# Kernel tuning notes

Measured on AMD Instinct MI355X. Metric: run time of the kernel, lower is better.

The kernel has to match this reference:

```python
import jax, jax.numpy as jnp
import numpy as np

ALPHA = 0.5  # config_param['alpha']


def setup_inputs() -> dict:
    key = jax.random.key(0)
    ks = jax.random.split(key, 10)
    B, T, N, E, H = 64, 20, 8192, 128, 128
    # sparse multi-hot basket indicators
    x = (jax.random.uniform(ks[0], (B, T, N)) < 0.01).astype(jnp.float32)
    seq_len = jax.random.randint(ks[1], (B,), 1, T + 1)  # pack_padded requires >=1
    A = jax.random.uniform(ks[2], (N, N), dtype=jnp.float32) * 0.01  # dense item-item adjacency
    W1 = jax.random.normal(ks[3], (E, N), dtype=jnp.float32) * 0.02
    b1 = jnp.zeros((E,), jnp.float32)
    W2 = jax.random.normal(ks[4], (E, N), dtype=jnp.float32) * 0.02
    b2 = jnp.zeros((E,), jnp.float32)
    W_ih = jax.random.normal(ks[5], (4 * H, E), dtype=jnp.float32) * 0.05
    W_hh = jax.random.normal(ks[6], (4 * H, H), dtype=jnp.float32) * 0.05
    b_ih = jnp.zeros((4 * H,), jnp.float32)
    b_hh = jnp.zeros((4 * H,), jnp.float32)
    W_out = jax.random.normal(ks[7], (N, H), dtype=jnp.float32) * 0.02
    I_B = jnp.ones((N,), jnp.float32) / N  # item_probs-style bias init
    threshold = jnp.array([0.005], jnp.float32)  # adj_matrix.mean()
    return dict(x=x, seq_len=seq_len, A=A, W1=W1, b1=b1, W2=W2, b2=b2,
                W_ih=W_ih, W_hh=W_hh, b_ih=b_ih, b_hh=b_hh,
                W_out=W_out, I_B=I_B, threshold=threshold)


def reference(x, seq_len, A, W1, b1, W2, b2, W_ih, W_hh, b_ih, b_hh, W_out, I_B, threshold):
    B, T, N = x.shape
    H = W_hh.shape[1]
    xf = x.reshape(B * T, N)
    # two basket encoders, elementwise max combine (dropout = identity in eval)
    e1 = jax.nn.relu(xf @ W1.T + b1)
    e2 = jax.nn.relu(xf @ W2.T + b2)
    basket = jnp.maximum(e1, e2).reshape(B, T, -1)  # [B, T, E]

    # 1-layer LSTM (torch gate order i,f,g,o); packed variable-length seqs
    # emulated by freezing (h, c) once t >= seq_len, so h_n matches pack_padded.
    valid = jnp.arange(T)[:, None] < seq_len[None, :]  # [T, B]
    xs = basket.transpose(1, 0, 2)                     # [T, B, E]
    b = b_ih + b_hh

    def step(carry, inp):
        h, c = carry
        x_t, v = inp
        gates = x_t @ W_ih.T + h @ W_hh.T + b
        i, f, g, o = jnp.split(gates, 4, axis=-1)
        c_new = jax.nn.sigmoid(f) * c + jax.nn.sigmoid(i) * jnp.tanh(g)
        h_new = jax.nn.sigmoid(o) * jnp.tanh(c_new)
        m = v[:, None]
        return (jnp.where(m, h_new, h), jnp.where(m, c_new, c)), None

    h0 = jnp.zeros((B, H), x.dtype)
    c0 = jnp.zeros((B, H), x.dtype)
    (h_n, _), _ = jax.lax.scan(step, (h0, c0), (xs, valid))

    p = jax.nn.sigmoid(h_n @ W_out.T)  # [B, N]
    # mm(p, diag(relu(I_B))) is algebraically an elementwise scale
    predict = (1.0 - ALPHA) * p + ALPHA * (p * jax.nn.relu(I_B) + jax.nn.relu(p @ A))
    return predict
```

## Files before the change

### kernel.cpp

```cpp
#include <hip/hip_runtime.h>
#include <hip/hip_bf16.h>
#include <stdint.h>

#define B_ 64
#define T_ 20
#define N_ 8192
#define E_ 128
#define H_ 128
#define G4 512
#define SPLITK 8

typedef short bf16x8 __attribute__((ext_vector_type(8)));
typedef float f32x4 __attribute__((ext_vector_type(4)));

__device__ __forceinline__ float sigmoidf_(float x){ return 1.0f/(1.0f+expf(-x)); }

__device__ __forceinline__ unsigned short f2bf(float f){
  union { float f; uint32_t u; } v; v.f = f;
  uint32_t u = v.u;
  uint32_t r = (u + 0x7FFFu + ((u >> 16) & 1u)) >> 16;
  return (unsigned short)r;
}
__device__ __forceinline__ uint32_t pk2(float a, float b){
  return (uint32_t)f2bf(a) | ((uint32_t)f2bf(b) << 16);
}
__device__ __forceinline__ float bf2f(unsigned short s){
  union { uint32_t u; float f; } v; v.u = ((uint32_t)s) << 16; return v.f;
}

__global__ void k_transpose(const float* __restrict__ W1, const float* __restrict__ W2,
                            unsigned short* __restrict__ W12T){
  __shared__ float t1[128][33];
  __shared__ float t2[128][33];
  int n0 = blockIdx.x * 32;
  int tid = threadIdx.x;
  int nl = tid & 31, eg = tid >> 5;
  for (int i = 0; i < 16; i++){
    int e = eg * 16 + i;
    t1[e][nl] = W1[(size_t)e*N_ + n0 + nl];
    t2[e][nl] = W2[(size_t)e*N_ + n0 + nl];
  }
  __syncthreads();
  for (int n = 0; n < 32; n++){
    float v = (tid < 128) ? t1[tid][n] : t2[tid-128][n];
    W12T[(size_t)(n0+n)*256 + tid] = f2bf(v);
  }
}

__global__ void k_mlp(const float* __restrict__ x, const int* __restrict__ seq_len,
                      const unsigned short* __restrict__ W12T, const float* __restrict__ b1,
                      const float* __restrict__ b2, float* __restrict__ basket){
  int bt = blockIdx.x;
  int b = bt / T_, t = bt % T_;
  int tid = threadIdx.x;
  if (t >= seq_len[b]){
    if (tid < 128) basket[(size_t)bt*E_ + tid] = 0.f;
    return;
  }
  __shared__ int idxs[1024];
  __shared__ int cnt;
  __shared__ float e2s[128];
  if (tid == 0) cnt = 0;
  __syncthreads();
  const float4* xr = (const float4*)(x + (size_t)bt * N_);
  for (int i = 0; i < 8; i++){
    float4 v = xr[i*256 + tid];
    int base = (i*256 + tid)*4;
    if (v.x != 0.f){ int q = atomicAdd(&cnt,1); idxs[q] = base;   }
    if (v.y != 0.f){ int q = atomicAdd(&cnt,1); idxs[q] = base+1; }
    if (v.z != 0.f){ int q = atomicAdd(&cnt,1); idxs[q] = base+2; }
    if (v.w != 0.f){ int q = atomicAdd(&cnt,1); idxs[q] = base+3; }
  }
  __syncthreads();
  int m = cnt; if (m > 1024) m = 1024;
  float acc = (tid < 128) ? b1[tid] : b2[tid-128];
  int i = 0;
  for (; i + 8 <= m; i += 8){
    int j0 = idxs[i+0], j1 = idxs[i+1], j2 = idxs[i+2], j3 = idxs[i+3];
    int j4 = idxs[i+4], j5 = idxs[i+5], j6 = idxs[i+6], j7 = idxs[i+7];
    float v0 = bf2f(W12T[(size_t)j0*256 + tid]);
    float v1 = bf2f(W12T[(size_t)j1*256 + tid]);
    float v2 = bf2f(W12T[(size_t)j2*256 + tid]);
    float v3 = bf2f(W12T[(size_t)j3*256 + tid]);
    float v4 = bf2f(W12T[(size_t)j4*256 + tid]);
    float v5 = bf2f(W12T[(size_t)j5*256 + tid]);
    float v6 = bf2f(W12T[(size_t)j6*256 + tid]);
    float v7 = bf2f(W12T[(size_t)j7*256 + tid]);
    acc += ((v0+v1)+(v2+v3)) + ((v4+v5)+(v6+v7));
  }
  for (; i < m; i++)
    acc += bf2f(W12T[(size_t)idxs[i]*256 + tid]);
  acc = fmaxf(acc, 0.f);
  if (tid >= 128) e2s[tid-128] = acc;
  __syncthreads();
  if (tid < 128) basket[(size_t)bt*E_ + tid] = fmaxf(acc, e2s[tid]);
}

__global__ void __launch_bounds__(512, 1)
k_lstmx(const int* __restrict__ seq_len, const float* __restrict__ basket,
        const float* __restrict__ W_ih, const float* __restrict__ b_ih,
        const float* __restrict__ b_hh, const float* __restrict__ W_hh,
        float* __restrict__ hn){
  int b = blockIdx.x;
  int L = seq_len[b];
  int j = threadIdx.x;
  __shared__ float bsk[T_][E_];
  __shared__ float XpL[T_][G4];
  __shared__ float hs[128];
  __shared__ float gs[512];
  for (int idx = j; idx < T_*E_; idx += 512)
    bsk[idx>>7][idx&127] = basket[((size_t)b*T_ + (idx>>7))*E_ + (idx&127)];
  __syncthreads();
  {
    float bias = b_ih[j] + b_hh[j];
    float accv[T_];
    #pragma unroll
    for (int tt = 0; tt < T_; tt++) accv[tt] = bias;
    const float4* wr = (const float4*)(W_ih + (size_t)j * E_);
    for (int k4 = 0; k4 < 32; k4++){
      float4 w = wr[k4];
      #pragma unroll
      for (int tt = 0; tt < T_; tt++){
        float4 h = *(const float4*)&bsk[tt][k4*4];
        accv[tt] += w.x*h.x + w.y*h.y + w.z*h.z + w.w*h.w;
      }
    }
    #pragma unroll
    for (int tt = 0; tt < T_; tt++) XpL[tt][j] = accv[tt];
  }
  float4 whh[32];
  const float4* wr2 = (const float4*)(W_hh + (size_t)j * H_);
  #pragma unroll
  for (int k = 0; k < 32; k++) whh[k] = wr2[k];
  if (j < 128) hs[j] = 0.f;
  float c = 0.f;
  __syncthreads();
  for (int t = 0; t < L; t++){
    float s0 = XpL[t][j], s1 = 0.f, s2 = 0.f, s3 = 0.f;
    #pragma unroll
    for (int k = 0; k < 32; k += 4){
      float4 w, h;
      w = whh[k+0]; h = *(const float4*)&hs[k*4+ 0]; s0 += w.x*h.x + w.y*h.y + w.z*h.z + w.w*h.w;
      w = whh[k+1]; h = *(const float4*)&hs[k*4+ 4]; s1 += w.x*h.x + w.y*h.y + w.z*h.z + w.w*h.w;
      w = whh[k+2]; h = *(const float4*)&hs[k*4+ 8]; s2 += w.x*h.x + w.y*h.y + w.z*h.z + w.w*h.w;
      w = whh[k+3]; h = *(const float4*)&hs[k*4+12]; s3 += w.x*h.x + w.y*h.y + w.z*h.z + w.w*h.w;
    }
    gs[j] = (s0 + s1) + (s2 + s3);
    __syncthreads();
    if (j < 128){
      float i_ = gs[j], f_ = gs[128+j], gg = gs[256+j], o_ = gs[384+j];
      c = sigmoidf_(f_)*c + sigmoidf_(i_)*tanhf(gg);
      hs[j] = sigmoidf_(o_)*tanhf(c);
    }
    __syncthreads();
  }
  if (j < 128) hn[(size_t)b*H_ + j] = hs[j];
}

__global__ void k_pout(const float* __restrict__ hn, const float* __restrict__ W_out,
                       unsigned short* __restrict__ pbf){
  __shared__ unsigned short hb[64*128];
  int tid = threadIdx.x;
  {
    int row = tid >> 2;
    int k16 = (tid & 3) * 32;
    const float4* hr = (const float4*)(hn + (size_t)row*H_ + k16);
    #pragma unroll
    for (int i = 0; i < 4; i++){
      float4 a = hr[i*2], bq = hr[i*2+1];
      uint4 u; u.x = pk2(a.x,a.y); u.y = pk2(a.z,a.w); u.z = pk2(bq.x,bq.y); u.w = pk2(bq.z,bq.w);
      int blk = (k16 >> 3) + i;
      *(uint4*)&hb[row*128 + ((blk ^ (row & 7)) * 8)] = u;
    }
  }
  __syncthreads();
  int w = tid >> 6, l = tid & 63;
  int n0 = blockIdx.x * 128;
  f32x4 acc[8];
  #pragma unroll
  for (int i = 0; i < 8; i++) acc[i] = (f32x4){0.f,0.f,0.f,0.f};
  int row = w*16 + (l & 15);
  #pragma unroll
  for (int ks = 0; ks < 4; ks++){
    int kk = ks*32 + (l >> 4)*8;
    int blk = kk >> 3;
    bf16x8 af = *(bf16x8*)&hb[row*128 + ((blk ^ (row & 7)) * 8)];
    #pragma unroll
    for (int nt = 0; nt < 8; nt++){
      int n = n0 + nt*16 + (l & 15);
      const float4* wp = (const float4*)(W_out + (size_t)n*H_ + kk);
      float4 wa = wp[0], wb = wp[1];
      union { uint4 u; bf16x8 v; } cc;
      cc.u.x = pk2(wa.x,wa.y); cc.u.y = pk2(wa.z,wa.w);
      cc.u.z = pk2(wb.x,wb.y); cc.u.w = pk2(wb.z,wb.w);
      acc[nt] = __builtin_amdgcn_mfma_f32_16x16x32_bf16(af, cc.v, acc[nt], 0, 0, 0);
    }
  }
  #pragma unroll
  for (int nt = 0; nt < 8; nt++){
    int n = n0 + nt*16 + (l & 15);
    #pragma unroll
    for (int r = 0; r < 4; r++){
      int rr = w*16 + (l >> 4)*4 + r;
      float pv = 1.f/(1.f + expf(-acc[nt][r]));
      pbf[(size_t)rr*N_ + n] = f2bf(pv);
    }
  }
}

#define ISSUE(a0,a1,a2,a3,pr,kb) do {                                          \
    pr = *(const uint4*)&pbf[(size_t)prow*N_ + (kb) + c8*8];                   \
    const float* bse = Ag + (size_t)(kb)*N_ + (size_t)kq*16*N_ + n0 + sn;      \
    a0.x = bse[0];              a0.y = bse[(size_t)N_];                        \
    a0.z = bse[(size_t)2*N_];   a0.w = bse[(size_t)3*N_];                      \
    a1.x = bse[(size_t)4*N_];   a1.y = bse[(size_t)5*N_];                      \
    a1.z = bse[(size_t)6*N_];   a1.w = bse[(size_t)7*N_];                      \
    a2.x = bse[(size_t)8*N_];   a2.y = bse[(size_t)9*N_];                      \
    a2.z = bse[(size_t)10*N_];  a2.w = bse[(size_t)11*N_];                     \
    a3.x = bse[(size_t)12*N_];  a3.y = bse[(size_t)13*N_];                     \
    a3.z = bse[(size_t)14*N_];  a3.w = bse[(size_t)15*N_];                     \
  } while(0)

#define STAGE(abf,ptb,a0,a1,a2,a3,pr) do {                                     \
    *(uint4*)&ptb[prow*64 + ((c8*8) ^ ((prow & 7)*8))] = pr;                   \
    uint2 u0, u1, u2, u3;                                                      \
    u0.x = pk2(a0.x,a0.y); u0.y = pk2(a0.z,a0.w);                              \
    u1.x = pk2(a1.x,a1.y); u1.y = pk2(a1.z,a1.w);                              \
    u2.x = pk2(a2.x,a2.y); u2.y = pk2(a2.z,a2.w);                              \
    u3.x = pk2(a3.x,a3.y); u3.y = pk2(a3.z,a3.w);                              \
    int kb0 = kq*16;                                                           \
    *(uint2*)&abf[sn*64 + ((kb0+ 0) ^ ((sn & 7)*8))] = u0;                     \
    *(uint2*)&abf[sn*64 + ((kb0+ 4) ^ ((sn & 7)*8))] = u1;                     \
    *(uint2*)&abf[sn*64 + ((kb0+ 8) ^ ((sn & 7)*8))] = u2;                     \
    *(uint2*)&abf[sn*64 + ((kb0+12) ^ ((sn & 7)*8))] = u3;                     \
  } while(0)

#define SYNC_AND() do {                                                        \
    asm volatile("s_waitcnt lgkmcnt(0)" ::: "memory");                         \
    __builtin_amdgcn_sched_barrier(0);                                         \
    __builtin_amdgcn_s_barrier();                                              \
    __builtin_amdgcn_sched_barrier(0);                                         \
  } while(0)

__global__ void __launch_bounds__(512, 4)
k_gemm(const unsigned short* __restrict__ pbf, const float* __restrict__ Ag,
       float* __restrict__ Cp){
  __shared__ unsigned short Abf0[128*64];
  __shared__ unsigned short Abf1[128*64];
  __shared__ unsigned short pt0[64*64];
  __shared__ unsigned short pt1[64*64];
  int tid = threadIdx.x;
  int nb = blockIdx.x & 63, ks = blockIdx.x >> 6;
  int n0 = nb * 128;
  int kbase = ks * (N_ / SPLITK);
  int sn = tid & 127, kq = tid >> 7;
  int prow = tid >> 3, c8 = tid & 7;
  int w = tid >> 6, l = tid & 63;
  int wm = w >> 2, wn = w & 3;
  f32x4 acc00 = {0,0,0,0}, acc01 = {0,0,0,0}, acc10 = {0,0,0,0}, acc11 = {0,0,0,0};
  float* Cout = Cp + (size_t)ks * (B_ * N_);
  const int NSTEP = (N_ / SPLITK) / 64;

  f32x4 aA0, aA1, aA2, aA3, aB0, aB1, aB2, aB3;
  uint4 pA, pB;

  auto compute = [&](const unsigned short* abf, const unsigned short* ptb){
    #pragma unroll
    for (int kc = 0; kc < 64; kc += 32){
      int ko = kc + (l >> 4)*8;
      bf16x8 af0, af1, bf0, bf1;
      {
        int r0 = wm*32 + (l & 15);
        int r1 = r0 + 16;
        af0 = *(const bf16x8*)&ptb[r0*64 + (ko ^ ((r0 & 7)*8))];
        af1 = *(const bf16x8*)&ptb[r1*64 + (ko ^ ((r1 & 7)*8))];
        int n0_ = wn*32 + (l & 15);
        int n1_ = n0_ + 16;
        bf0 = *(const bf16x8*)&abf[n0_*64 + (ko ^ ((n0_ & 7)*8))];
        bf1 = *(const bf16x8*)&abf[n1_*64 + (ko ^ ((n1_ & 7)*8))];
      }
      acc00 = __builtin_amdgcn_mfma_f32_16x16x32_bf16(af0, bf0, acc00, 0, 0, 0);
      acc01 = __builtin_amdgcn_mfma_f32_16x16x32_bf16(af0, bf1, acc01, 0, 0, 0);
      acc10 = __builtin_amdgcn_mfma_f32_16x16x32_bf16(af1, bf0, acc10, 0, 0, 0);
      acc11 = __builtin_amdgcn_mfma_f32_16x16x32_bf16(af1, bf1, acc11, 0, 0, 0);
    }
  };

  ISSUE(aA0,aA1,aA2,aA3,pA, kbase);
  for (int s = 0; s < NSTEP; s += 2){
    if (s + 1 < NSTEP) ISSUE(aB0,aB1,aB2,aB3,pB, kbase + (s+1)*64);
    STAGE(Abf0, pt0, aA0,aA1,aA2,aA3, pA);
    SYNC_AND();
    compute(Abf0, pt0);
    if (s + 2 < NSTEP) ISSUE(aA0,aA1,aA2,aA3,pA, kbase + (s+2)*64);
    STAGE(Abf1, pt1, aB0,aB1,aB2,aB3, pB);
    SYNC_AND();
    compute(Abf1, pt1);
  }

  {
    int n_a = n0 + wn*32 + (l & 15);
    int n_b = n_a + 16;
    int rbase = wm*32 + (l >> 4)*4;
    #pragma unroll
    for (int r = 0; r < 4; r++){
      Cout[(size_t)(rbase + r)*N_ + n_a]      = acc00[r];
      Cout[(size_t)(rbase + r)*N_ + n_b]      = acc01[r];
      Cout[(size_t)(rbase + 16 + r)*N_ + n_a] = acc10[r];
      Cout[(size_t)(rbase + 16 + r)*N_ + n_b] = acc11[r];
    }
  }
}

__global__ void k_final(const unsigned short* __restrict__ pbf, const float* __restrict__ Cp,
                        const float* __restrict__ I_B, float* __restrict__ out){
  int idx = blockIdx.x*256 + threadIdx.x;
  ushort4 pu = ((const ushort4*)pbf)[idx];
  float4 cv = {0.f, 0.f, 0.f, 0.f};
  #pragma unroll
  for (int s = 0; s < SPLITK; s++){
    float4 v = ((const float4*)(Cp + (size_t)s * (B_ * N_)))[idx];
    cv.x += v.x; cv.y += v.y; cv.z += v.z; cv.w += v.w;
  }
  int n = (idx*4) & (N_-1);
  float4 ib = *(const float4*)&I_B[n];
  float4 o;
  float p0 = bf2f(pu.x), p1 = bf2f(pu.y), p2 = bf2f(pu.z), p3 = bf2f(pu.w);
  o.x = 0.5f*p0 + 0.5f*(p0*fmaxf(ib.x,0.f) + fmaxf(cv.x,0.f));
  o.y = 0.5f*p1 + 0.5f*(p1*fmaxf(ib.y,0.f) + fmaxf(cv.y,0.f));
  o.z = 0.5f*p2 + 0.5f*(p2*fmaxf(ib.z,0.f) + fmaxf(cv.z,0.f));
  o.w = 0.5f*p3 + 0.5f*(p3*fmaxf(ib.w,0.f) + fmaxf(cv.w,0.f));
  ((float4*)out)[idx] = o;
}

extern "C" void kernel_launch(void* const* d_in, const int* in_sizes, int n_in,
                              void* d_out, int out_size, void* d_ws, size_t ws_size,
                              hipStream_t stream) {
  const float* x     = (const float*)d_in[0];
  const int*   seq   = (const int*)  d_in[1];
  const float* A     = (const float*)d_in[2];
  const float* W1    = (const float*)d_in[3];
  const float* b1    = (const float*)d_in[4];
  const float* W2    = (const float*)d_in[5];
  const float* b2    = (const float*)d_in[6];
  const float* W_ih  = (const float*)d_in[7];
  const float* W_hh  = (const float*)d_in[8];
  const float* b_ih  = (const float*)d_in[9];
  const float* b_hh  = (const float*)d_in[10];
  const float* W_out = (const float*)d_in[11];
  const float* I_B   = (const float*)d_in[12];
  float* out = (float*)d_out;

  float* ws = (float*)d_ws;
  unsigned short* W12T = (unsigned short*)ws;
  float* basket = ws + 1048576;
  float* hn     = basket + 163840;
  float* Cp     = hn + 8192;
  unsigned short* pbf = (unsigned short*)(Cp + 4194304);

  k_transpose<<<256, 256, 0, stream>>>(W1, W2, W12T);
  k_mlp      <<<1280,256, 0, stream>>>(x, seq, W12T, b1, b2, basket);
  k_lstmx    <<<64,  512, 0, stream>>>(seq, basket, W_ih, b_ih, b_hh, W_hh, hn);
  k_pout     <<<64,  256, 0, stream>>>(hn, W_out, pbf);
  k_gemm     <<<64*SPLITK, 512, 0, stream>>>(pbf, A, Cp);
  k_final    <<<512, 256, 0, stream>>>(pbf, Cp, I_B, out);
}
```

Measured before the change: 149.8 us.

## Split LSTM into MFMA input-projection GEMM and MFMA recurrent kernel

The LSTM input projection moves out of the per-batch kernel into a separate bf16 MFMA GEMM over all B*T rows, writing Xp to workspace. The recurrence now runs with 16 batches per block on 4 blocks, using MFMA with bf16 W_hh fragments held in registers. A bf16 copy of W_hh is produced inside the existing prep kernel. This replaces the scalar fp32 dot products in the serial LSTM loop with matrix instructions, at the cost of an extra launch, bf16 rounding of h and W_hh, and only 4 blocks running the recurrence.

```diff
diff --git a/kernel.cpp b/kernel.cpp
--- a/kernel.cpp
+++ b/kernel.cpp
@@ -28,12 +28,21 @@
   union { uint32_t u; float f; } v; v.u = ((uint32_t)s) << 16; return v.f;
 }
 
-__global__ void k_transpose(const float* __restrict__ W1, const float* __restrict__ W2,
-                            unsigned short* __restrict__ W12T){
+__global__ void k_prep(const float* __restrict__ W1, const float* __restrict__ W2,
+                       unsigned short* __restrict__ W12T,
+                       const float* __restrict__ W_hh, unsigned short* __restrict__ W_hhB){
+  int blk = blockIdx.x;
+  int tid = threadIdx.x;
+  if (blk >= 256){
+    int base = (blk - 256)*4096 + tid;
+    #pragma unroll
+    for (int i = 0; i < 16; i++)
+      W_hhB[base + i*256] = f2bf(W_hh[base + i*256]);
+    return;
+  }
   __shared__ float t1[128][33];
   __shared__ float t2[128][33];
-  int n0 = blockIdx.x * 32;
-  int tid = threadIdx.x;
+  int n0 = blk * 32;
   int nl = tid & 31, eg = tid >> 5;
   for (int i = 0; i < 16; i++){
     int e = eg * 16 + i;
@@ -96,65 +105,135 @@
   if (tid < 128) basket[(size_t)bt*E_ + tid] = fmaxf(acc, e2s[tid]);
 }
 
+__global__ void k_xgemm(const float* __restrict__ basket, const float* __restrict__ W_ih,
+                        const float* __restrict__ b_ih, const float* __restrict__ b_hh,
+                        float* __restrict__ Xp){
+  __shared__ unsigned short hb[64*128];
+  int tid = threadIdx.x;
+  int rt = blockIdx.x;
+  int ct = blockIdx.y;
+  {
+    int row = tid >> 2;
+    int k16 = (tid & 3) * 32;
+    const float4* hr = (const float4*)(basket + ((size_t)rt*64 + row)*E_ + k16);
+    #pragma unroll
+    for (int i = 0; i < 4; i++){
+      float4 a = hr[i*2], bq = hr[i*2+1];
+      uint4 u; u.x = pk2(a.x,a.y); u.y = pk2(a.z,a.w); u.z = pk2(bq.x,bq.y); u.w = pk2(bq.z,bq.w);
+      int blk = (k16 >> 3) + i;
+      *(uint4*)&hb[row*128 + ((blk ^ (row & 7)) * 8)] = u;
+    }
+  }
+  __syncthreads();
+  int w = tid >> 6, l = tid & 63;
+  int n0 = ct * 128;
+  f32x4 acc[8];
+  #pragma unroll
+  for (int i = 0; i < 8; i++) acc[i] = (f32x4){0.f,0.f,0.f,0.f};
+  int row = w*16 + (l & 15);
+  #pragma unroll
+  for (int ks = 0; ks < 4; ks++){
+    int kk = ks*32 + (l >> 4)*8;
+    int blk = kk >> 3;
+    bf16x8 af = *(bf16x8*)&hb[row*128 + ((blk ^ (row & 7)) * 8)];
+    #pragma unroll
+    for (int nt = 0; nt < 8; nt++){
+      int n = n0 + nt*16 + (l & 15);
+      const float4* wp = (const float4*)(W_ih + (size_t)n*E_ + kk);
+      float4 wa = wp[0], wb = wp[1];
+      union { uint4 u; bf16x8 v; } cc;
+      cc.u.x = pk2(wa.x,wa.y); cc.u.y = pk2(wa.z,wa.w);
+      cc.u.z = pk2(wb.x,wb.y); cc.u.w = pk2(wb.z,wb.w);
+      acc[nt] = __builtin_amdgcn_mfma_f32_16x16x32_bf16(af, cc.v, acc[nt], 0, 0, 0);
+    }
+  }
+  #pragma unroll
+  for (int nt = 0; nt < 8; nt++){
+    int n = n0 + nt*16 + (l & 15);
+    float bias = b_ih[n] + b_hh[n];
+    #pragma unroll
+    for (int r = 0; r < 4; r++){
+      int rr = w*16 + (l >> 4)*4 + r;
+      Xp[((size_t)rt*64 + rr)*G4 + n] = acc[nt][r] + bias;
+    }
+  }
+}
+
 __global__ void __launch_bounds__(512, 1)
-k_lstmx(const int* __restrict__ seq_len, const float* __restrict__ basket,
-        const float* __restrict__ W_ih, const float* __restrict__ b_ih,
-        const float* __restrict__ b_hh, const float* __restrict__ W_hh,
-        float* __restrict__ hn){
-  int b = blockIdx.x;
-  int L = seq_len[b];
-  int j = threadIdx.x;
-  __shared__ float bsk[T_][E_];
-  __shared__ float XpL[T_][G4];
-  __shared__ float hs[128];
-  __shared__ float gs[512];
-  for (int idx = j; idx < T_*E_; idx += 512)
-    bsk[idx>>7][idx&127] = basket[((size_t)b*T_ + (idx>>7))*E_ + (idx&127)];
-  __syncthreads();
-  {
-    float bias = b_ih[j] + b_hh[j];
-    float accv[T_];
-    #pragma unroll
-    for (int tt = 0; tt < T_; tt++) accv[tt] = bias;
-    const float4* wr = (const float4*)(W_ih + (size_t)j * E_);
-    for (int k4 = 0; k4 < 32; k4++){
-      float4 w = wr[k4];
-      #pragma unroll
-      for (int tt = 0; tt < T_; tt++){
-        float4 h = *(const float4*)&bsk[tt][k4*4];
-        accv[tt] += w.x*h.x + w.y*h.y + w.z*h.z + w.w*h.w;
-      }
-    }
-    #pragma unroll
-    for (int tt = 0; tt < T_; tt++) XpL[tt][j] = accv[tt];
-  }
-  float4 whh[32];
-  const float4* wr2 = (const float4*)(W_hh + (size_t)j * H_);
-  #pragma unroll
-  for (int k = 0; k < 32; k++) whh[k] = wr2[k];
-  if (j < 128) hs[j] = 0.f;
-  float c = 0.f;
-  __syncthreads();
-  for (int t = 0; t < L; t++){
-    float s0 = XpL[t][j], s1 = 0.f, s2 = 0.f, s3 = 0.f;
-    #pragma unroll
-    for (int k = 0; k < 32; k += 4){
-      float4 w, h;
-      w = whh[k+0]; h = *(const float4*)&hs[k*4+ 0]; s0 += w.x*h.x + w.y*h.y + w.z*h.z + w.w*h.w;
-      w = whh[k+1]; h = *(const float4*)&hs[k*4+ 4]; s1 += w.x*h.x + w.y*h.y + w.z*h.z + w.w*h.w;
-      w = whh[k+2]; h = *(const float4*)&hs[k*4+ 8]; s2 += w.x*h.x + w.y*h.y + w.z*h.z + w.w*h.w;
-      w = whh[k+3]; h = *(const float4*)&hs[k*4+12]; s3 += w.x*h.x + w.y*h.y + w.z*h.z + w.w*h.w;
-    }
-    gs[j] = (s0 + s1) + (s2 + s3);
+k_lstm(const int* __restrict__ seq_len, const float* __restrict__ Xp,
+       const unsigned short* __restrict__ W_hhB, float* __restrict__ hn){
+  __shared__ unsigned short Hs[16*128];
+  int tid = threadIdx.x;
+  int w = tid >> 6, l = tid & 63;
+  int b0 = blockIdx.x * 16;
+  int c16 = l & 15, r16 = l >> 4;
+  int jcol = w*16 + c16;
+  bf16x8 wf[4][4];
+  #pragma unroll
+  for (int g = 0; g < 4; g++){
+    int n = g*128 + jcol;
+    #pragma unroll
+    for (int kc = 0; kc < 4; kc++)
+      wf[g][kc] = *(const bf16x8*)&W_hhB[(size_t)n*128 + kc*32 + r16*8];
+  }
+  int L0 = seq_len[b0 + r16*4 + 0];
+  int L1 = seq_len[b0 + r16*4 + 1];
+  int L2 = seq_len[b0 + r16*4 + 2];
+  int L3 = seq_len[b0 + r16*4 + 3];
+  float c0=0.f,c1=0.f,c2=0.f,c3=0.f;
+  float h0=0.f,h1=0.f,h2=0.f,h3=0.f;
+  for (int i = tid; i < 16*128; i += 512) Hs[i] = 0;
+  __syncthreads();
+  for (int t = 0; t < T_; t++){
+    int arow = c16;
+    int sw = (arow & 7);
+    bf16x8 af0 = *(const bf16x8*)&Hs[arow*128 + (((0*4 + r16) ^ sw)*8)];
+    bf16x8 af1 = *(const bf16x8*)&Hs[arow*128 + (((1*4 + r16) ^ sw)*8)];
+    bf16x8 af2 = *(const bf16x8*)&Hs[arow*128 + (((2*4 + r16) ^ sw)*8)];
+    bf16x8 af3 = *(const bf16x8*)&Hs[arow*128 + (((3*4 + r16) ^ sw)*8)];
+    f32x4 aI = {0.f,0.f,0.f,0.f}, aF = {0.f,0.f,0.f,0.f};
+    f32x4 aG = {0.f,0.f,0.f,0.f}, aO = {0.f,0.f,0.f,0.f};
+    aI = __builtin_amdgcn_mfma_f32_16x16x32_bf16(af0, wf[0][0], aI, 0,0,0);
+    aI = __builtin_amdgcn_mfma_f32_16x16x32_bf16(af1, wf[0][1], aI, 0,0,0);
+    aI = __builtin_amdgcn_mfma_f32_16x16x32_bf16(af2, wf[0][2], aI, 0,0,0);
+    aI = __builtin_amdgcn_mfma_f32_16x16x32_bf16(af3, wf[0][3], aI, 0,0,0);
+    aF = __builtin_amdgcn_mfma_f32_16x16x32_bf16(af0, wf[1][0], aF, 0,0,0);
+    aF = __builtin_amdgcn_mfma_f32_16x16x32_bf16(af1, wf[1][1], aF, 0,0,0);
+    aF = __builtin_amdgcn_mfma_f32_16x16x32_bf16(af2, wf[1][2], aF, 0,0,0);
+    aF = __builtin_amdgcn_mfma_f32_16x16x32_bf16(af3, wf[1][3], aF, 0,0,0);
+    aG = __builtin_amdgcn_mfma_f32_16x16x32_bf16(af0, wf[2][0], aG, 0,0,0);
+    aG = __builtin_amdgcn_mfma_f32_16x16x32_bf16(af1, wf[2][1], aG, 0,0,0);
+    aG = __builtin_amdgcn_mfma_f32_16x16x32_bf16(af2, wf[2][2], aG, 0,0,0);
+    aG = __builtin_amdgcn_mfma_f32_16x16x32_bf16(af3, wf[2][3], aG, 0,0,0);
+    aO = __builtin_amdgcn_mfma_f32_16x16x32_bf16(af0, wf[3][0], aO, 0,0,0);
+    aO = __builtin_amdgcn_mfma_f32_16x16x32_bf16(af1, wf[3][1], aO, 0,0,0);
+    aO = __builtin_amdgcn_mfma_f32_16x16x32_bf16(af2, wf[3][2], aO, 0,0,0);
+    aO = __builtin_amdgcn_mfma_f32_16x16x32_bf16(af3, wf[3][3], aO, 0,0,0);
     __syncthreads();
-    if (j < 128){
-      float i_ = gs[j], f_ = gs[128+j], gg = gs[256+j], o_ = gs[384+j];
-      c = sigmoidf_(f_)*c + sigmoidf_(i_)*tanhf(gg);
-      hs[j] = sigmoidf_(o_)*tanhf(c);
-    }
+    #define ROWSTEP(r, cc, hh, LL) {                                        \
+      int b = b0 + r16*4 + r;                                               \
+      size_t xb = ((size_t)b*T_ + t)*G4 + jcol;                             \
+      float zi = aI[r] + Xp[xb];                                            \
+      float zf = aF[r] + Xp[xb + 128];                                      \
+      float zg = aG[r] + Xp[xb + 256];                                      \
+      float zo = aO[r] + Xp[xb + 384];                                      \
+      float cn = sigmoidf_(zf)*cc + sigmoidf_(zi)*tanhf(zg);                \
+      float hv = sigmoidf_(zo)*tanhf(cn);                                   \
+      if (t < LL){ cc = cn; hh = hv; }                                      \
+      int brow = r16*4 + r;                                                 \
+      Hs[brow*128 + ((((jcol>>3) ^ (brow & 7)))*8) + (l & 7)] = f2bf(hh);   \
+    }
+    ROWSTEP(0, c0, h0, L0)
+    ROWSTEP(1, c1, h1, L1)
+    ROWSTEP(2, c2, h2, L2)
+    ROWSTEP(3, c3, h3, L3)
+    #undef ROWSTEP
     __syncthreads();
   }
-  if (j < 128) hn[(size_t)b*H_ + j] = hs[j];
+  hn[(size_t)(b0 + r16*4 + 0)*H_ + jcol] = h0;
+  hn[(size_t)(b0 + r16*4 + 1)*H_ + jcol] = h1;
+  hn[(size_t)(b0 + r16*4 + 2)*H_ + jcol] = h2;
+  hn[(size_t)(b0 + r16*4 + 3)*H_ + jcol] = h3;
 }
 
 __global__ void k_pout(const float* __restrict__ hn, const float* __restrict__ W_out,
@@ -352,16 +431,19 @@
   float* out = (float*)d_out;
 
   float* ws = (float*)d_ws;
-  unsigned short* W12T = (unsigned short*)ws;
-  float* basket = ws + 1048576;
-  float* hn     = basket + 163840;
+  unsigned short* W12T  = (unsigned short*)ws;
+  unsigned short* W_hhB = (unsigned short*)(ws + 1048576);
+  float* basket = ws + 1048576 + 32768;
+  float* Xp     = basket + 163840;
+  float* hn     = Xp + 655360;
   float* Cp     = hn + 8192;
   unsigned short* pbf = (unsigned short*)(Cp + 4194304);
 
-  k_transpose<<<256, 256, 0, stream>>>(W1, W2, W12T);
-  k_mlp      <<<1280,256, 0, stream>>>(x, seq, W12T, b1, b2, basket);
-  k_lstmx    <<<64,  512, 0, stream>>>(seq, basket, W_ih, b_ih, b_hh, W_hh, hn);
-  k_pout     <<<64,  256, 0, stream>>>(hn, W_out, pbf);
-  k_gemm     <<<64*SPLITK, 512, 0, stream>>>(pbf, A, Cp);
-  k_final    <<<512, 256, 0, stream>>>(pbf, Cp, I_B, out);
-}
+  k_prep  <<<272, 256, 0, stream>>>(W1, W2, W12T, W_hh, W_hhB);
+  k_mlp   <<<1280,256, 0, stream>>>(x, seq, W12T, b1, b2, basket);
+  k_xgemm <<<dim3(20,4), 256, 0, stream>>>(basket, W_ih, b_ih, b_hh, Xp);
+  k_lstm  <<<4,   512, 0, stream>>>(seq, Xp, W_hhB, hn);
+  k_pout  <<<64,  256, 0, stream>>>(hn, W_out, pbf);
+  k_gemm  <<<64*SPLITK, 512, 0, stream>>>(pbf, A, Cp);
+  k_final <<<512, 256, 0, stream>>>(pbf, Cp, I_B, out);
+}
```

Result: slower. 171.9 us (+14.7%).

## Fuse front-end kernels into one cooperative kernel with grid syncs

Applied to the files above, without the earlier changes.

Merges the weight transpose, sparse MLP encoder, LSTM and output projection kernels into a single cooperative kernel of 256 blocks, separated by grid-wide syncs. The aim is to remove three kernel launch gaps and their serialization. The MLP stage now has each 512-thread block handle five (b,t) rows, with two half-blocks splitting the nonzero list and reducing through shared memory. The later stages run on only 64 blocks while the rest sit idle, and the grid syncs add their own cost. Index capacity drops from 1024 to 512 nonzeros per row.

```diff
diff --git a/kernel.cpp b/kernel.cpp
--- a/kernel.cpp
+++ b/kernel.cpp
@@ -1,6 +1,8 @@
 #include <hip/hip_runtime.h>
-#include <hip/hip_bf16.h>
+#include <hip/hip_cooperative_groups.h>
 #include <stdint.h>
+
+namespace cg = cooperative_groups;
 
 #define B_ 64
 #define T_ 20
@@ -28,182 +30,208 @@
   union { uint32_t u; float f; } v; v.u = ((uint32_t)s) << 16; return v.f;
 }
 
-__global__ void k_transpose(const float* __restrict__ W1, const float* __restrict__ W2,
-                            unsigned short* __restrict__ W12T){
-  __shared__ float t1[128][33];
-  __shared__ float t2[128][33];
-  int n0 = blockIdx.x * 32;
-  int tid = threadIdx.x;
-  int nl = tid & 31, eg = tid >> 5;
-  for (int i = 0; i < 16; i++){
-    int e = eg * 16 + i;
-    t1[e][nl] = W1[(size_t)e*N_ + n0 + nl];
-    t2[e][nl] = W2[(size_t)e*N_ + n0 + nl];
-  }
-  __syncthreads();
-  for (int n = 0; n < 32; n++){
-    float v = (tid < 128) ? t1[tid][n] : t2[tid-128][n];
-    W12T[(size_t)(n0+n)*256 + tid] = f2bf(v);
-  }
-}
-
-__global__ void k_mlp(const float* __restrict__ x, const int* __restrict__ seq_len,
-                      const unsigned short* __restrict__ W12T, const float* __restrict__ b1,
-                      const float* __restrict__ b2, float* __restrict__ basket){
-  int bt = blockIdx.x;
-  int b = bt / T_, t = bt % T_;
-  int tid = threadIdx.x;
-  if (t >= seq_len[b]){
-    if (tid < 128) basket[(size_t)bt*E_ + tid] = 0.f;
-    return;
-  }
-  __shared__ int idxs[1024];
-  __shared__ int cnt;
-  __shared__ float e2s[128];
-  if (tid == 0) cnt = 0;
-  __syncthreads();
-  const float4* xr = (const float4*)(x + (size_t)bt * N_);
-  for (int i = 0; i < 8; i++){
-    float4 v = xr[i*256 + tid];
-    int base = (i*256 + tid)*4;
-    if (v.x != 0.f){ int q = atomicAdd(&cnt,1); idxs[q] = base;   }
-    if (v.y != 0.f){ int q = atomicAdd(&cnt,1); idxs[q] = base+1; }
-    if (v.z != 0.f){ int q = atomicAdd(&cnt,1); idxs[q] = base+2; }
-    if (v.w != 0.f){ int q = atomicAdd(&cnt,1); idxs[q] = base+3; }
-  }
-  __syncthreads();
-  int m = cnt; if (m > 1024) m = 1024;
-  float acc = (tid < 128) ? b1[tid] : b2[tid-128];
-  int i = 0;
-  for (; i + 8 <= m; i += 8){
-    int j0 = idxs[i+0], j1 = idxs[i+1], j2 = idxs[i+2], j3 = idxs[i+3];
-    int j4 = idxs[i+4], j5 = idxs[i+5], j6 = idxs[i+6], j7 = idxs[i+7];
-    float v0 = bf2f(W12T[(size_t)j0*256 + tid]);
-    float v1 = bf2f(W12T[(size_t)j1*256 + tid]);
-    float v2 = bf2f(W12T[(size_t)j2*256 + tid]);
-    float v3 = bf2f(W12T[(size_t)j3*256 + tid]);
-    float v4 = bf2f(W12T[(size_t)j4*256 + tid]);
-    float v5 = bf2f(W12T[(size_t)j5*256 + tid]);
-    float v6 = bf2f(W12T[(size_t)j6*256 + tid]);
-    float v7 = bf2f(W12T[(size_t)j7*256 + tid]);
-    acc += ((v0+v1)+(v2+v3)) + ((v4+v5)+(v6+v7));
-  }
-  for (; i < m; i++)
-    acc += bf2f(W12T[(size_t)idxs[i]*256 + tid]);
-  acc = fmaxf(acc, 0.f);
-  if (tid >= 128) e2s[tid-128] = acc;
-  __syncthreads();
-  if (tid < 128) basket[(size_t)bt*E_ + tid] = fmaxf(acc, e2s[tid]);
-}
-
-__global__ void __launch_bounds__(512, 1)
-k_lstmx(const int* __restrict__ seq_len, const float* __restrict__ basket,
+__global__ void __launch_bounds__(512, 2)
+k_front(const float* __restrict__ W1, const float* __restrict__ W2,
+        const float* __restrict__ x, const int* __restrict__ seq_len,
+        const float* __restrict__ b1, const float* __restrict__ b2,
         const float* __restrict__ W_ih, const float* __restrict__ b_ih,
         const float* __restrict__ b_hh, const float* __restrict__ W_hh,
-        float* __restrict__ hn){
-  int b = blockIdx.x;
-  int L = seq_len[b];
-  int j = threadIdx.x;
-  __shared__ float bsk[T_][E_];
-  __shared__ float XpL[T_][G4];
-  __shared__ float hs[128];
-  __shared__ float gs[512];
-  for (int idx = j; idx < T_*E_; idx += 512)
-    bsk[idx>>7][idx&127] = basket[((size_t)b*T_ + (idx>>7))*E_ + (idx&127)];
-  __syncthreads();
+        const float* __restrict__ W_out,
+        unsigned short* __restrict__ W12T, float* __restrict__ basket,
+        float* __restrict__ hn, unsigned short* __restrict__ pbf){
+  __shared__ char sm[53760] __attribute__((aligned(16)));
+  cg::grid_group grid = cg::this_grid();
+  const int blk = blockIdx.x;
+  const int tid = threadIdx.x;
+
   {
-    float bias = b_ih[j] + b_hh[j];
-    float accv[T_];
-    #pragma unroll
-    for (int tt = 0; tt < T_; tt++) accv[tt] = bias;
-    const float4* wr = (const float4*)(W_ih + (size_t)j * E_);
-    for (int k4 = 0; k4 < 32; k4++){
-      float4 w = wr[k4];
-      #pragma unroll
-      for (int tt = 0; tt < T_; tt++){
-        float4 h = *(const float4*)&bsk[tt][k4*4];
-        accv[tt] += w.x*h.x + w.y*h.y + w.z*h.z + w.w*h.w;
-      }
-    }
-    #pragma unroll
-    for (int tt = 0; tt < T_; tt++) XpL[tt][j] = accv[tt];
-  }
-  float4 whh[32];
-  const float4* wr2 = (const float4*)(W_hh + (size_t)j * H_);
-  #pragma unroll
-  for (int k = 0; k < 32; k++) whh[k] = wr2[k];
-  if (j < 128) hs[j] = 0.f;
-  float c = 0.f;
-  __syncthreads();
-  for (int t = 0; t < L; t++){
-    float s0 = XpL[t][j], s1 = 0.f, s2 = 0.f, s3 = 0.f;
-    #pragma unroll
-    for (int k = 0; k < 32; k += 4){
-      float4 w, h;
-      w = whh[k+0]; h = *(const float4*)&hs[k*4+ 0]; s0 += w.x*h.x + w.y*h.y + w.z*h.z + w.w*h.w;
-      w = whh[k+1]; h = *(const float4*)&hs[k*4+ 4]; s1 += w.x*h.x + w.y*h.y + w.z*h.z + w.w*h.w;
-      w = whh[k+2]; h = *(const float4*)&hs[k*4+ 8]; s2 += w.x*h.x + w.y*h.y + w.z*h.z + w.w*h.w;
-      w = whh[k+3]; h = *(const float4*)&hs[k*4+12]; s3 += w.x*h.x + w.y*h.y + w.z*h.z + w.w*h.w;
-    }
-    gs[j] = (s0 + s1) + (s2 + s3);
+    float (*t1)[33] = (float(*)[33])sm;
+    float (*t2)[33] = (float(*)[33])(sm + 128*33*4);
+    int n0 = blk * 32;
+    int nl = tid & 31, eg = tid >> 5;
+    #pragma unroll
+    for (int i = 0; i < 8; i++){
+      int e = eg*8 + i;
+      t1[e][nl] = W1[(size_t)e*N_ + n0 + nl];
+      t2[e][nl] = W2[(size_t)e*N_ + n0 + nl];
+    }
     __syncthreads();
-    if (j < 128){
-      float i_ = gs[j], f_ = gs[128+j], gg = gs[256+j], o_ = gs[384+j];
-      c = sigmoidf_(f_)*c + sigmoidf_(i_)*tanhf(gg);
-      hs[j] = sigmoidf_(o_)*tanhf(c);
-    }
+    int c = tid & 255, hq = tid >> 8;
+    #pragma unroll
+    for (int nn = 0; nn < 16; nn++){
+      int n = hq*16 + nn;
+      float v = (c < 128) ? t1[c][n] : t2[c-128][n];
+      W12T[(size_t)(n0+n)*256 + c] = f2bf(v);
+    }
+  }
+  grid.sync();
+
+  {
+    int*   idxs = (int*)sm;
+    int*   cntp = (int*)(sm + 2048);
+    float* sums = (float*)(sm + 2064);
+    int e = tid & 255, hf = tid >> 8;
+    for (int it = 0; it < 5; it++){
+      int bt = it*256 + blk;
+      int b = bt / T_, t = bt % T_;
+      bool valid = (t < seq_len[b]);
+      __syncthreads();
+      if (valid && tid == 0) *cntp = 0;
+      __syncthreads();
+      if (valid){
+        const float4* xr = (const float4*)(x + (size_t)bt * N_);
+        #pragma unroll
+        for (int i = 0; i < 4; i++){
+          float4 v = xr[i*512 + tid];
+          int base = (i*512 + tid)*4;
+          if (v.x != 0.f){ int q = atomicAdd(cntp,1); if (q < 512) idxs[q] = base;   }
+          if (v.y != 0.f){ int q = atomicAdd(cntp,1); if (q < 512) idxs[q] = base+1; }
+          if (v.z != 0.f){ int q = atomicAdd(cntp,1); if (q < 512) idxs[q] = base+2; }
+          if (v.w != 0.f){ int q = atomicAdd(cntp,1); if (q < 512) idxs[q] = base+3; }
+        }
+      }
+      __syncthreads();
+      if (valid){
+        int m = *cntp; if (m > 512) m = 512;
+        float acc = (hf == 0) ? ((e < 128) ? b1[e] : b2[e-128]) : 0.f;
+        int i = hf;
+        for (; i + 14 < m; i += 16){
+          int j0 = idxs[i+ 0], j1 = idxs[i+ 2], j2 = idxs[i+ 4], j3 = idxs[i+ 6];
+          int j4 = idxs[i+ 8], j5 = idxs[i+10], j6 = idxs[i+12], j7 = idxs[i+14];
+          float v0 = bf2f(W12T[(size_t)j0*256 + e]);
+          float v1 = bf2f(W12T[(size_t)j1*256 + e]);
+          float v2 = bf2f(W12T[(size_t)j2*256 + e]);
+          float v3 = bf2f(W12T[(size_t)j3*256 + e]);
+          float v4 = bf2f(W12T[(size_t)j4*256 + e]);
+          float v5 = bf2f(W12T[(size_t)j5*256 + e]);
+          float v6 = bf2f(W12T[(size_t)j6*256 + e]);
+          float v7 = bf2f(W12T[(size_t)j7*256 + e]);
+          acc += ((v0+v1)+(v2+v3)) + ((v4+v5)+(v6+v7));
+        }
+        for (; i < m; i += 2)
+          acc += bf2f(W12T[(size_t)idxs[i]*256 + e]);
+        sums[hf*256 + e] = acc;
+      }
+      __syncthreads();
+      if (tid < 128){
+        if (valid){
+          float r1 = fmaxf(sums[tid]       + sums[256+tid], 0.f);
+          float r2 = fmaxf(sums[128+tid]   + sums[384+tid], 0.f);
+          basket[(size_t)bt*E_ + tid] = fmaxf(r1, r2);
+        } else {
+          basket[(size_t)bt*E_ + tid] = 0.f;
+        }
+      }
+    }
+  }
+  grid.sync();
+
+  if (blk < 64){
+    float (*bsk)[E_] = (float(*)[E_])sm;
+    float (*XpL)[G4] = (float(*)[G4])(sm + 10240);
+    float* hs = (float*)(sm + 51200);
+    float* gs = (float*)(sm + 51712);
+    int b = blk;
+    int L = seq_len[b];
+    int j = tid;
+    for (int idx = j; idx < T_*E_; idx += 512)
+      bsk[idx>>7][idx&127] = basket[((size_t)b*T_ + (idx>>7))*E_ + (idx&127)];
     __syncthreads();
-  }
-  if (j < 128) hn[(size_t)b*H_ + j] = hs[j];
-}
-
-__global__ void k_pout(const float* __restrict__ hn, const float* __restrict__ W_out,
-                       unsigned short* __restrict__ pbf){
-  __shared__ unsigned short hb[64*128];
-  int tid = threadIdx.x;
-  {
-    int row = tid >> 2;
-    int k16 = (tid & 3) * 32;
-    const float4* hr = (const float4*)(hn + (size_t)row*H_ + k16);
-    #pragma unroll
-    for (int i = 0; i < 4; i++){
-      float4 a = hr[i*2], bq = hr[i*2+1];
-      uint4 u; u.x = pk2(a.x,a.y); u.y = pk2(a.z,a.w); u.z = pk2(bq.x,bq.y); u.w = pk2(bq.z,bq.w);
-      int blk = (k16 >> 3) + i;
-      *(uint4*)&hb[row*128 + ((blk ^ (row & 7)) * 8)] = u;
-    }
-  }
-  __syncthreads();
-  int w = tid >> 6, l = tid & 63;
-  int n0 = blockIdx.x * 128;
-  f32x4 acc[8];
-  #pragma unroll
-  for (int i = 0; i < 8; i++) acc[i] = (f32x4){0.f,0.f,0.f,0.f};
-  int row = w*16 + (l & 15);
-  #pragma unroll
-  for (int ks = 0; ks < 4; ks++){
-    int kk = ks*32 + (l >> 4)*8;
-    int blk = kk >> 3;
-    bf16x8 af = *(bf16x8*)&hb[row*128 + ((blk ^ (row & 7)) * 8)];
-    #pragma unroll
-    for (int nt = 0; nt < 8; nt++){
-      int n = n0 + nt*16 + (l & 15);
-      const float4* wp = (const float4*)(W_out + (size_t)n*H_ + kk);
-      float4 wa = wp[0], wb = wp[1];
-      union { uint4 u; bf16x8 v; } cc;
-      cc.u.x = pk2(wa.x,wa.y); cc.u.y = pk2(wa.z,wa.w);
-      cc.u.z = pk2(wb.x,wb.y); cc.u.w = pk2(wb.z,wb.w);
-      acc[nt] = __builtin_amdgcn_mfma_f32_16x16x32_bf16(af, cc.v, acc[nt], 0, 0, 0);
-    }
-  }
-  #pragma unroll
-  for (int nt = 0; nt < 8; nt++){
-    int n = n0 + nt*16 + (l & 15);
-    #pragma unroll
-    for (int r = 0; r < 4; r++){
-      int rr = w*16 + (l >> 4)*4 + r;
-      float pv = 1.f/(1.f + expf(-acc[nt][r]));
-      pbf[(size_t)rr*N_ + n] = f2bf(pv);
+    {
+      float bias = b_ih[j] + b_hh[j];
+      float accv[T_];
+      #pragma unroll
+      for (int tt = 0; tt < T_; tt++) accv[tt] = bias;
+      const float4* wr = (const float4*)(W_ih + (size_t)j * E_);
+      for (int k4 = 0; k4 < 32; k4++){
+        float4 w = wr[k4];
+        #pragma unroll
+        for (int tt = 0; tt < T_; tt++){
+          float4 h = *(const float4*)&bsk[tt][k4*4];
+          accv[tt] += w.x*h.x + w.y*h.y + w.z*h.z + w.w*h.w;
+        }
+      }
+      #pragma unroll
+      for (int tt = 0; tt < T_; tt++) XpL[tt][j] = accv[tt];
+    }
+    float4 whh[32];
+    const float4* wr2 = (const float4*)(W_hh + (size_t)j * H_);
+    #pragma unroll
+    for (int k = 0; k < 32; k++) whh[k] = wr2[k];
+    if (j < 128) hs[j] = 0.f;
+    float c = 0.f;
+    __syncthreads();
+    for (int t = 0; t < L; t++){
+      float s0 = XpL[t][j], s1 = 0.f, s2 = 0.f, s3 = 0.f;
+      #pragma unroll
+      for (int k = 0; k < 32; k += 4){
+        float4 w, h;
+        w = whh[k+0]; h = *(const float4*)&hs[k*4+ 0]; s0 += w.x*h.x + w.y*h.y + w.z*h.z + w.w*h.w;
+        w = whh[k+1]; h = *(const float4*)&hs[k*4+ 4]; s1 += w.x*h.x + w.y*h.y + w.z*h.z + w.w*h.w;
+        w = whh[k+2]; h = *(const float4*)&hs[k*4+ 8]; s2 += w.x*h.x + w.y*h.y + w.z*h.z + w.w*h.w;
+        w = whh[k+3]; h = *(const float4*)&hs[k*4+12]; s3 += w.x*h.x + w.y*h.y + w.z*h.z + w.w*h.w;
+      }
+      gs[j] = (s0 + s1) + (s2 + s3);
+      __syncthreads();
+      if (j < 128){
+        float i_ = gs[j], f_ = gs[128+j], gg = gs[256+j], o_ = gs[384+j];
+        c = sigmoidf_(f_)*c + sigmoidf_(i_)*tanhf(gg);
+        hs[j] = sigmoidf_(o_)*tanhf(c);
+      }
+      __syncthreads();
+    }
+    if (j < 128) hn[(size_t)b*H_ + j] = hs[j];
+  }
+  grid.sync();
+
+  if (blk < 64){
+    unsigned short* hb = (unsigned short*)sm;
+    if (tid < 256){
+      int row = tid >> 2;
+      int k16 = (tid & 3) * 32;
+      const float4* hr = (const float4*)(hn + (size_t)row*H_ + k16);
+      #pragma unroll
+      for (int i = 0; i < 4; i++){
+        float4 a = hr[i*2], bq = hr[i*2+1];
+        uint4 u; u.x = pk2(a.x,a.y); u.y = pk2(a.z,a.w); u.z = pk2(bq.x,bq.y); u.w = pk2(bq.z,bq.w);
+        int bb = (k16 >> 3) + i;
+        *(uint4*)&hb[row*128 + ((bb ^ (row & 7)) * 8)] = u;
+      }
+    }
+    __syncthreads();
+    if (tid < 256){
+      int w = tid >> 6, l = tid & 63;
+      int n0 = blk * 128;
+      f32x4 acc[8];
+      #pragma unroll
+      for (int i = 0; i < 8; i++) acc[i] = (f32x4){0.f,0.f,0.f,0.f};
+      int row = w*16 + (l & 15);
+      #pragma unroll
+      for (int ks = 0; ks < 4; ks++){
+        int kk = ks*32 + (l >> 4)*8;
+        int bb = kk >> 3;
+        bf16x8 af = *(bf16x8*)&hb[row*128 + ((bb ^ (row & 7)) * 8)];
+        #pragma unroll
+        for (int nt = 0; nt < 8; nt++){
+          int n = n0 + nt*16 + (l & 15);
+          const float4* wp = (const float4*)(W_out + (size_t)n*H_ + kk);
+          float4 wa = wp[0], wb = wp[1];
+          union { uint4 u; bf16x8 v; } cc;
+          cc.u.x = pk2(wa.x,wa.y); cc.u.y = pk2(wa.z,wa.w);
+          cc.u.z = pk2(wb.x,wb.y); cc.u.w = pk2(wb.z,wb.w);
+          acc[nt] = __builtin_amdgcn_mfma_f32_16x16x32_bf16(af, cc.v, acc[nt], 0, 0, 0);
+        }
+      }
+      #pragma unroll
+      for (int nt = 0; nt < 8; nt++){
+        int n = n0 + nt*16 + (l & 15);
+        #pragma unroll
+        for (int r = 0; r < 4; r++){
+          int rr = w*16 + (l >> 4)*4 + r;
+          float pv = 1.f/(1.f + expf(-acc[nt][r]));
+          pbf[(size_t)rr*N_ + n] = f2bf(pv);
+        }
+      }
     }
   }
 }
@@ -358,10 +386,11 @@
   float* Cp     = hn + 8192;
   unsigned short* pbf = (unsigned short*)(Cp + 4194304);
 
-  k_transpose<<<256, 256, 0, stream>>>(W1, W2, W12T);
-  k_mlp      <<<1280,256, 0, stream>>>(x, seq, W12T, b1, b2, basket);
-  k_lstmx    <<<64,  512, 0, stream>>>(seq, basket, W_ih, b_ih, b_hh, W_hh, hn);
-  k_pout     <<<64,  256, 0, stream>>>(hn, W_out, pbf);
-  k_gemm     <<<64*SPLITK, 512, 0, stream>>>(pbf, A, Cp);
-  k_final    <<<512, 256, 0, stream>>>(pbf, Cp, I_B, out);
-}
+  void* args[] = {(void*)&W1, (void*)&W2, (void*)&x, (void*)&seq,
+                  (void*)&b1, (void*)&b2, (void*)&W_ih, (void*)&b_ih,
+                  (void*)&b_hh, (void*)&W_hh, (void*)&W_out,
+                  (void*)&W12T, (void*)&basket, (void*)&hn, (void*)&pbf};
+  hipLaunchCooperativeKernel((void*)k_front, dim3(256), dim3(512), args, 0, stream);
+  k_gemm <<<64*SPLITK, 512, 0, stream>>>(pbf, A, Cp);
+  k_final<<<512, 256, 0, stream>>>(pbf, Cp, I_B, out);
+}
```

Result: slower. 238.9 us (+59.5%).

## Split LSTM input projection into separate MFMA GEMM kernel and prefetch Xp

Applied to the files above, without the earlier changes.

Moves the input-to-gate projection for all B*T rows out of the per-batch LSTM kernel into a separate bf16 MFMA GEMM launched across 80 blocks. The recurrent kernel then only streams precomputed Xp rows from global memory, prefetching the next timestep. This takes the serial fp32 projection off the 64-block LSTM critical path, at the cost of an extra launch, a global round trip for Xp, and bf16 rounding of the projection inputs.

```diff
diff --git a/kernel.cpp b/kernel.cpp
--- a/kernel.cpp
+++ b/kernel.cpp
@@ -96,47 +96,79 @@
   if (tid < 128) basket[(size_t)bt*E_ + tid] = fmaxf(acc, e2s[tid]);
 }
 
+__global__ void k_xgemm(const float* __restrict__ basket, const float* __restrict__ W_ih,
+                        const float* __restrict__ b_ih, const float* __restrict__ b_hh,
+                        float* __restrict__ Xp){
+  __shared__ unsigned short hb[64*128];
+  int tid = threadIdx.x;
+  int rt = blockIdx.x;
+  int ct = blockIdx.y;
+  {
+    int row = tid >> 2;
+    int k16 = (tid & 3) * 32;
+    const float4* hr = (const float4*)(basket + ((size_t)rt*64 + row)*E_ + k16);
+    #pragma unroll
+    for (int i = 0; i < 4; i++){
+      float4 a = hr[i*2], bq = hr[i*2+1];
+      uint4 u; u.x = pk2(a.x,a.y); u.y = pk2(a.z,a.w); u.z = pk2(bq.x,bq.y); u.w = pk2(bq.z,bq.w);
+      int blk = (k16 >> 3) + i;
+      *(uint4*)&hb[row*128 + ((blk ^ (row & 7)) * 8)] = u;
+    }
+  }
+  __syncthreads();
+  int w = tid >> 6, l = tid & 63;
+  int n0 = ct * 128;
+  f32x4 acc[8];
+  #pragma unroll
+  for (int i = 0; i < 8; i++) acc[i] = (f32x4){0.f,0.f,0.f,0.f};
+  int row = w*16 + (l & 15);
+  #pragma unroll
+  for (int ks = 0; ks < 4; ks++){
+    int kk = ks*32 + (l >> 4)*8;
+    int blk = kk >> 3;
+    bf16x8 af = *(bf16x8*)&hb[row*128 + ((blk ^ (row & 7)) * 8)];
+    #pragma unroll
+    for (int nt = 0; nt < 8; nt++){
+      int n = n0 + nt*16 + (l & 15);
+      const float4* wp = (const float4*)(W_ih + (size_t)n*E_ + kk);
+      float4 wa = wp[0], wb = wp[1];
+      union { uint4 u; bf16x8 v; } cc;
+      cc.u.x = pk2(wa.x,wa.y); cc.u.y = pk2(wa.z,wa.w);
+      cc.u.z = pk2(wb.x,wb.y); cc.u.w = pk2(wb.z,wb.w);
+      acc[nt] = __builtin_amdgcn_mfma_f32_16x16x32_bf16(af, cc.v, acc[nt], 0, 0, 0);
+    }
+  }
+  #pragma unroll
+  for (int nt = 0; nt < 8; nt++){
+    int n = n0 + nt*16 + (l & 15);
+    float bias = b_ih[n] + b_hh[n];
+    #pragma unroll
+    for (int r = 0; r < 4; r++){
+      int rr = w*16 + (l >> 4)*4 + r;
+      Xp[((size_t)rt*64 + rr)*G4 + n] = acc[nt][r] + bias;
+    }
+  }
+}
+
 __global__ void __launch_bounds__(512, 1)
-k_lstmx(const int* __restrict__ seq_len, const float* __restrict__ basket,
-        const float* __restrict__ W_ih, const float* __restrict__ b_ih,
-        const float* __restrict__ b_hh, const float* __restrict__ W_hh,
-        float* __restrict__ hn){
+k_lstm64(const int* __restrict__ seq_len, const float* __restrict__ Xp,
+         const float* __restrict__ W_hh, float* __restrict__ hn){
   int b = blockIdx.x;
   int L = seq_len[b];
   int j = threadIdx.x;
-  __shared__ float bsk[T_][E_];
-  __shared__ float XpL[T_][G4];
+  float4 whh[32];
+  const float4* wr = (const float4*)(W_hh + (size_t)j * H_);
+  #pragma unroll
+  for (int k = 0; k < 32; k++) whh[k] = wr[k];
   __shared__ float hs[128];
   __shared__ float gs[512];
-  for (int idx = j; idx < T_*E_; idx += 512)
-    bsk[idx>>7][idx&127] = basket[((size_t)b*T_ + (idx>>7))*E_ + (idx&127)];
-  __syncthreads();
-  {
-    float bias = b_ih[j] + b_hh[j];
-    float accv[T_];
-    #pragma unroll
-    for (int tt = 0; tt < T_; tt++) accv[tt] = bias;
-    const float4* wr = (const float4*)(W_ih + (size_t)j * E_);
-    for (int k4 = 0; k4 < 32; k4++){
-      float4 w = wr[k4];
-      #pragma unroll
-      for (int tt = 0; tt < T_; tt++){
-        float4 h = *(const float4*)&bsk[tt][k4*4];
-        accv[tt] += w.x*h.x + w.y*h.y + w.z*h.z + w.w*h.w;
-      }
-    }
-    #pragma unroll
-    for (int tt = 0; tt < T_; tt++) XpL[tt][j] = accv[tt];
-  }
-  float4 whh[32];
-  const float4* wr2 = (const float4*)(W_hh + (size_t)j * H_);
-  #pragma unroll
-  for (int k = 0; k < 32; k++) whh[k] = wr2[k];
   if (j < 128) hs[j] = 0.f;
   float c = 0.f;
+  float xp_cur = Xp[(size_t)b*T_*G4 + j];
   __syncthreads();
   for (int t = 0; t < L; t++){
-    float s0 = XpL[t][j], s1 = 0.f, s2 = 0.f, s3 = 0.f;
+    float xp_next = (t + 1 < L) ? Xp[((size_t)b*T_ + t + 1)*G4 + j] : 0.f;
+    float s0 = xp_cur, s1 = 0.f, s2 = 0.f, s3 = 0.f;
     #pragma unroll
     for (int k = 0; k < 32; k += 4){
       float4 w, h;
@@ -153,6 +185,7 @@
       hs[j] = sigmoidf_(o_)*tanhf(c);
     }
     __syncthreads();
+    xp_cur = xp_next;
   }
   if (j < 128) hn[(size_t)b*H_ + j] = hs[j];
 }
@@ -354,13 +387,15 @@
   float* ws = (float*)d_ws;
   unsigned short* W12T = (unsigned short*)ws;
   float* basket = ws + 1048576;
-  float* hn     = basket + 163840;
+  float* Xp     = basket + 163840;
+  float* hn     = Xp + 655360;
   float* Cp     = hn + 8192;
   unsigned short* pbf = (unsigned short*)(Cp + 4194304);
 
   k_transpose<<<256, 256, 0, stream>>>(W1, W2, W12T);
   k_mlp      <<<1280,256, 0, stream>>>(x, seq, W12T, b1, b2, basket);
-  k_lstmx    <<<64,  512, 0, stream>>>(seq, basket, W_ih, b_ih, b_hh, W_hh, hn);
+  k_xgemm    <<<dim3(20,4), 256, 0, stream>>>(basket, W_ih, b_ih, b_hh, Xp);
+  k_lstm64   <<<64,  512, 0, stream>>>(seq, Xp, W_hh, hn);
   k_pout     <<<64,  256, 0, stream>>>(hn, W_out, pbf);
   k_gemm     <<<64*SPLITK, 512, 0, stream>>>(pbf, A, Cp);
   k_final    <<<512, 256, 0, stream>>>(pbf, Cp, I_B, out);
```

Result: no change. 152.1 us (+1.6%).
